# Kernel optimization log

Measured on AMD Instinct MI355X. Metric: run time of the kernel, lower is better.

Reference implementation:

```python
import jax, jax.numpy as jnp
import numpy as np

B, C, H, W = 16, 256, 64, 64
K, HID, ITERS, EPS = 4, 512, 3, 1e-8


def _ln(x, g, b, eps=1e-5):
    m = jnp.mean(x, axis=-1, keepdims=True)
    v = jnp.mean((x - m) ** 2, axis=-1, keepdims=True)
    return (x - m) * jax.lax.rsqrt(v + eps) * g + b


def setup_inputs() -> dict:
    key = jax.random.key(0)
    ks = jax.random.split(key, 24)

    def lin(k, o, i):
        lim = np.sqrt(6.0 / (o + i)).astype(np.float32)
        return jax.random.uniform(k, (o, i), jnp.float32, -lim, lim)

    return {
        "x": jax.random.normal(ks[0], (B, C, H, W), jnp.float32),
        "noise": jax.random.normal(ks[1], (B, K, C), jnp.float32),
        "slot_mu": jax.random.normal(ks[2], (1, 1, C), jnp.float32),
        "slot_log_sigma": jnp.zeros((1, 1, C), jnp.float32),
        "ln_in_g": jnp.ones((C,)), "ln_in_b": jnp.zeros((C,)),
        "ln_sl_g": jnp.ones((C,)), "ln_sl_b": jnp.zeros((C,)),
        "ln_mlp_g": jnp.ones((C,)), "ln_mlp_b": jnp.zeros((C,)),
        "Wq": lin(ks[3], C, C), "bq": jnp.zeros((C,)),
        "Wk": lin(ks[4], C, C), "bk": jnp.zeros((C,)),
        "Wv": lin(ks[5], C, C), "bv": jnp.zeros((C,)),
        "Wu": lin(ks[6], C, 2 * C), "bu": jnp.zeros((C,)),
        "W1": lin(ks[7], HID, C), "b1": jnp.zeros((HID,)),
        "W2": lin(ks[8], C, HID), "b2": jnp.zeros((C,)),
        "We1": lin(ks[9], C // 2, C), "be1": jnp.zeros((C // 2,)),
        "We2": lin(ks[10], 1, C // 2), "be2": jnp.zeros((1,)),
    }


def reference(x, noise, slot_mu, slot_log_sigma, ln_in_g, ln_in_b, ln_sl_g, ln_sl_b,
              ln_mlp_g, ln_mlp_b, Wq, bq, Wk, bk, Wv, bv, Wu, bu, W1, b1, W2, b2,
              We1, be1, We2, be2):
    # b c h w -> b (h w) c
    xn = x.reshape(B, C, H * W).transpose(0, 2, 1)
    xn = _ln(xn, ln_in_g, ln_in_b)
    # k, v depend only on xn; hoisted out of the loop (same math)
    k = jnp.einsum('bnc,dc->bnd', xn, Wk) + bk
    v = jnp.einsum('bnc,dc->bnd', xn, Wv) + bv
    scale = C ** (-0.5)
    slots = slot_mu + jnp.exp(slot_log_sigma) * noise
    for _ in range(ITERS):
        prev = slots
        s = _ln(slots, ln_sl_g, ln_sl_b)
        q = jnp.einsum('bkc,dc->bkd', s, Wq) + bq
        attn = jax.nn.softmax(jnp.einsum('bkc,bnc->bkn', q, k) * scale, axis=1)
        w = attn / (jnp.sum(attn, axis=-1, keepdims=True) + EPS)
        updates = jnp.einsum('bkn,bnc->bkc', w, v)
        combined = jnp.concatenate([prev, updates], axis=-1)  # (B,K,2C)
        slots = jnp.einsum('bkc,dc->bkd', combined, Wu) + bu + prev
        m = _ln(slots, ln_mlp_g, ln_mlp_b)
        h = jax.nn.gelu(jnp.einsum('bkc,hc->bkh', m, W1) + b1, approximate=False)
        slots = slots + jnp.einsum('bkh,ch->bkc', h, W2) + b2
    e = jax.nn.gelu(jnp.einsum('bkc,dc->bkd', slots, We1) + be1, approximate=False)
    slot_weights = jax.nn.sigmoid(jnp.einsum('bkd,od->bko', e, We2) + be2)[..., 0]
    return slots, slot_weights
```

## Files before the change

kernel.cpp:

```cpp
#include <hip/hip_runtime.h>
#include <math.h>

#define B_    16
#define C_    256
#define NPIX  4096
#define K_    4
#define HID_  512
#define ITERS_ 3
#define NROWS (B_*NPIX)
#define EPS_  1e-8f

__device__ __forceinline__ float gelu_f(float x) {
    return 0.5f * x * (1.0f + erff(x * 0.70710678118654752f));
}

__device__ __forceinline__ unsigned short f2bf(float x) {
    union { float f; unsigned u; } v; v.f = x;
    unsigned r = v.u + 0x7fffu + ((v.u >> 16) & 1u);
    return (unsigned short)(r >> 16);
}
__device__ __forceinline__ float bflo(unsigned u) {
    union { unsigned u; float f; } v; v.u = u << 16; return v.f;
}
__device__ __forceinline__ float bfhi(unsigned u) {
    union { unsigned u; float f; } v; v.u = u & 0xffff0000u; return v.f;
}
__device__ __forceinline__ float4 shfl_xor4(float4 v, int m) {
    v.x = __shfl_xor(v.x, m); v.y = __shfl_xor(v.y, m);
    v.z = __shfl_xor(v.z, m); v.w = __shfl_xor(v.w, m);
    return v;
}
__device__ __forceinline__ void fma4(float4& a, const float4 w, const float4 s) {
    a.x = fmaf(w.x, s.x, a.x); a.y = fmaf(w.y, s.y, a.y);
    a.z = fmaf(w.z, s.z, a.z); a.w = fmaf(w.w, s.w, a.w);
}
__device__ __forceinline__ float hsum4(const float4 a) {
    return (a.x + a.y) + (a.z + a.w);
}

__device__ __forceinline__ void redpair256(float a, float b, int tid, int q,
                                           float* r8, float& o1, float& o2) {
    if (q == 0) {
        #pragma unroll
        for (int m = 1; m <= 32; m <<= 1) { a += __shfl_xor(a, m); b += __shfl_xor(b, m); }
        if ((tid & 63) == 0) { r8[(tid >> 6) * 2] = a; r8[(tid >> 6) * 2 + 1] = b; }
    }
    __syncthreads();
    o1 = r8[0] + r8[2] + r8[4] + r8[6];
    o2 = r8[1] + r8[3] + r8[5] + r8[7];
    __syncthreads();
}

__global__ __launch_bounds__(256) void prep_pack_kernel(
    const float* __restrict__ Wu, const float* __restrict__ W1,
    const float* __restrict__ W2, const float* __restrict__ We1,
    const float* __restrict__ Wq, const float* __restrict__ bk,
    const float* __restrict__ bq,
    float4* __restrict__ WuC4, float4* __restrict__ W14,
    float4* __restrict__ W24, float4* __restrict__ We14,
    float* __restrict__ wqoff) {
    __shared__ float r4[4];
    int i = blockIdx.x * 256 + threadIdx.x;
    if (blockIdx.x == 352) {
        int c = threadIdx.x;
        float s = 0.f;
        for (int dd = 0; dd < 256; ++dd) s = fmaf(Wq[dd * 256 + c], bk[dd], s);
        wqoff[c] = s;
        float p = bq[c] * bk[c];
        #pragma unroll
        for (int m = 1; m <= 32; m <<= 1) p += __shfl_xor(p, m);
        if ((c & 63) == 0) r4[c >> 6] = p;
        __syncthreads();
        if (c == 0) wqoff[256] = r4[0] + r4[1] + r4[2] + r4[3];
        return;
    }
    if (i < 16384) {
        int c4 = i >> 8, dd = i & 255;
        WuC4[i] = *(const float4*)&Wu[dd * 512 + c4 * 4];
    } else if (i < 49152) {
        int j = i - 16384; int c4 = j >> 9, h = j & 511;
        W14[j] = *(const float4*)&W1[h * 256 + c4 * 4];
    } else if (i < 81920) {
        int j = i - 49152; int h4 = j >> 8, dd = j & 255;
        W24[j] = *(const float4*)&W2[dd * 512 + h4 * 4];
    } else {
        int j = i - 81920; int c4 = j >> 7, e = j & 127;
        We14[j] = *(const float4*)&We1[e * 256 + c4 * 4];
    }
}

__global__ __launch_bounds__(256) void prep_compose_kernel(
    const float* __restrict__ Wu, const float* __restrict__ Wv,
    const float* __restrict__ Wk, const float* __restrict__ Wq,
    const float* __restrict__ bv, const float* __restrict__ bq,
    float4* __restrict__ WuC4, float4* __restrict__ Wqk4,
    float* __restrict__ bv2, float* __restrict__ bqk) {
    __shared__ float wur[256], wkc[256];
    __shared__ float ldsA[256], ldsB[256];
    __shared__ float r1[4], r2[4];
    const int d = blockIdx.x, c = threadIdx.x;
    wur[c] = Wu[d * 512 + 256 + c];
    wkc[c] = Wk[c * 256 + d];
    __syncthreads();
    float a = 0.f, b = 0.f;
    #pragma unroll 4
    for (int e = 0; e < 256; ++e) {
        a = fmaf(wur[e], Wv[e * 256 + c], a);
        b = fmaf(wkc[e], Wq[e * 256 + c], b);
    }
    ldsA[c] = a; ldsB[c] = b;
    float p1 = wur[c] * bv[c], p2 = wkc[c] * bq[c];
    #pragma unroll
    for (int m = 1; m <= 32; m <<= 1) { p1 += __shfl_xor(p1, m); p2 += __shfl_xor(p2, m); }
    if ((c & 63) == 0) { r1[c >> 6] = p1; r2[c >> 6] = p2; }
    __syncthreads();
    if (c < 64) {
        float4 qa = { ldsA[4 * c], ldsA[4 * c + 1], ldsA[4 * c + 2], ldsA[4 * c + 3] };
        float4 qb = { ldsB[4 * c], ldsB[4 * c + 1], ldsB[4 * c + 2], ldsB[4 * c + 3] };
        WuC4[(64 + c) * 256 + d] = qa;
        Wqk4[c * 256 + d] = qb;
    }
    if (c == 0) {
        bv2[d] = r1[0] + r1[1] + r1[2] + r1[3];
        bqk[d] = r2[0] + r2[1] + r2[2] + r2[3];
    }
}

__global__ __launch_bounds__(256) void xn_fused_kernel(
    const float* __restrict__ x, const float* __restrict__ g, const float* __restrict__ bta,
    unsigned short* __restrict__ xnb) {
    __shared__ float tile[256][65];
    __shared__ float sg[256], sb[256];
    __shared__ float red1[256], red2[256];
    __shared__ float smean[64], srstd[64];
    const int tid = threadIdx.x;
    const int nt = blockIdx.x << 6, b = blockIdx.y;

    sg[tid] = g[tid]; sb[tid] = bta[tid];
    #pragma unroll
    for (int r = 0; r < 64; ++r) {
        int idx = tid + (r << 8);
        int c_l = idx >> 6, n_l = idx & 63;
        tile[c_l][n_l] = x[(size_t)(b * C_ + c_l) * NPIX + nt + n_l];
    }
    __syncthreads();
    {
        int cq = tid >> 6, n_l = tid & 63;
        float s = 0.f, s2 = 0.f;
        #pragma unroll 8
        for (int c = cq * 64; c < cq * 64 + 64; ++c) {
            float v = tile[c][n_l];
            s += v; s2 += v * v;
        }
        red1[tid] = s; red2[tid] = s2;
    }
    __syncthreads();
    if (tid < 64) {
        float s  = red1[tid] + red1[tid + 64] + red1[tid + 128] + red1[tid + 192];
        float s2 = red2[tid] + red2[tid + 64] + red2[tid + 128] + red2[tid + 192];
        float m = s * (1.0f / C_);
        smean[tid] = m;
        srstd[tid] = rsqrtf(s2 * (1.0f / C_) - m * m + 1e-5f);
    }
    __syncthreads();
    #pragma unroll
    for (int r = 0; r < 32; ++r) {
        int idx = tid + (r << 8);
        int n_l = idx >> 7, cp = idx & 127;
        int c0 = cp << 1;
        float mn = smean[n_l], rs = srstd[n_l];
        float v0 = (tile[c0][n_l] - mn) * rs * sg[c0] + sb[c0];
        float v1 = (tile[c0 + 1][n_l] - mn) * rs * sg[c0 + 1] + sb[c0 + 1];
        ushort2 o; o.x = f2bf(v0); o.y = f2bf(v1);
        *reinterpret_cast<ushort2*>(&xnb[((size_t)(b * NPIX + nt + n_l)) * C_ + c0]) = o;
    }
}


__device__ __forceinline__ void ln_qt_1024(
    float v, int tid, int d, int q, int r,
    const float* __restrict__ g_sl, const float* __restrict__ b_sl,
    const float4* __restrict__ Wqk4, const float* __restrict__ bqk,
    const float* __restrict__ wqoff,
    float* __restrict__ qtbuf, float* __restrict__ qoffbuf,
    float* snorm, float* pq, float* r8) {
    float a = (q == 0) ? v : 0.f;
    float sm, s2;
    redpair256(a, a * v, tid, q, r8, sm, s2);
    if (q == 0) {
        float m = sm * (1.f / C_);
        float rs = rsqrtf(s2 * (1.f / C_) - m * m + 1e-5f);
        snorm[d] = (v - m) * rs * g_sl[d] + b_sl[d];
    }
    __syncthreads();
    {
        const float4* sn4 = (const float4*)snorm;
        float4 a0 = {0,0,0,0}, a1 = {0,0,0,0};
        int c4b = q << 4;
        #pragma unroll
        for (int i = 0; i < 16; i += 2) {
            fma4(a0, Wqk4[(c4b + i) * 256 + d], sn4[c4b + i]);
            fma4(a1, Wqk4[(c4b + i + 1) * 256 + d], sn4[c4b + i + 1]);
        }
        pq[q * 256 + d] = hsum4(a0) + hsum4(a1);
    }
    float p = (q == 0) ? snorm[d] * wqoff[d] : 0.f;
    float qo, dum;
    redpair256(p, 0.f, tid, q, r8, qo, dum);
    if (tid == 0) qoffbuf[r] = qo + wqoff[256];
    if (q == 0)
        qtbuf[r * C_ + d] = pq[d] + pq[256 + d] + pq[512 + d] + pq[768 + d] + bqk[d];
}

__global__ __launch_bounds__(1024) void slot_init_q_kernel(
    const float* __restrict__ noise, const float* __restrict__ mu,
    const float* __restrict__ log_sigma,
    const float* __restrict__ g_sl, const float* __restrict__ b_sl,
    const float4* __restrict__ Wqk4, const float* __restrict__ bqk,
    const float* __restrict__ wqoff,
    float* __restrict__ slots, float* __restrict__ qtbuf, float* __restrict__ qoffbuf,
    float* __restrict__ usum, float* __restrict__ denom) {
    __shared__ __align__(16) float snorm[256];
    __shared__ float pq[1024];
    __shared__ float r8[8];
    int tid = threadIdx.x;
    int d = tid & 255, q = tid >> 8;
    int r = blockIdx.x;
    float v = 0.f;
    if (q == 0) {
        v = mu[d] + expf(log_sigma[d]) * noise[r * C_ + d];
        slots[r * C_ + d] = v;
        usum[r * C_ + d] = 0.f;
    }
    if (tid == 0) denom[r] = 0.f;
    ln_qt_1024(v, tid, d, q, r, g_sl, b_sl, Wqk4, bqk, wqoff,
               qtbuf, qoffbuf, snorm, pq, r8);
}

__device__ __forceinline__ float slot_update_body(
    int tid, int d, int q, int r, const float* __restrict__ slots,
    float* __restrict__ usum, float* __restrict__ denom,
    const float* __restrict__ bv2,
    const float4* __restrict__ WuC4, const float* __restrict__ bu,
    const float* __restrict__ g_mlp, const float* __restrict__ b_mlp,
    const float4* __restrict__ W14, const float* __restrict__ b1,
    const float4* __restrict__ W24, const float* __restrict__ b2,
    float* comb, float* pq, float* mrow, float* hrow,
    float* r8, float* s_denom, float* s_scale) {
    float uv = 0.f, prev = 0.f;
    if (q == 0) {
        uv = usum[r * C_ + d];
        usum[r * C_ + d] = 0.f;
        prev = slots[r * C_ + d];
    }
    if (tid == 0) {
        float dv = denom[r];
        *s_denom = dv + EPS_;
        *s_scale = dv / (dv + EPS_);
        denom[r] = 0.f;
    }
    __syncthreads();
    if (q == 0) {
        comb[d] = prev;
        comb[256 + d] = uv / *s_denom;
    }
    __syncthreads();
    const float4* cb4 = (const float4*)comb;
    {
        float4 a0 = {0,0,0,0}, a1 = {0,0,0,0}, a2 = {0,0,0,0}, a3 = {0,0,0,0};
        int c4b = q << 5;
        #pragma unroll
        for (int i = 0; i < 32; i += 4) {
            float4 w0 = WuC4[(c4b + i + 0) * 256 + d];
            float4 w1 = WuC4[(c4b + i + 1) * 256 + d];
            float4 w2 = WuC4[(c4b + i + 2) * 256 + d];
            float4 w3 = WuC4[(c4b + i + 3) * 256 + d];
            fma4(a0, w0, cb4[c4b + i + 0]); fma4(a1, w1, cb4[c4b + i + 1]);
            fma4(a2, w2, cb4[c4b + i + 2]); fma4(a3, w3, cb4[c4b + i + 3]);
        }
        pq[q * 256 + d] = (hsum4(a0) + hsum4(a1)) + (hsum4(a2) + hsum4(a3));
    }
    __syncthreads();
    float nv = 0.f, aa = 0.f;
    if (q == 0) {
        nv = pq[d] + pq[256 + d] + pq[512 + d] + pq[768 + d]
           + bu[d] + prev + (*s_scale) * bv2[d];
        aa = nv;
    }
    float sm, s2;
    redpair256(aa, aa * nv, tid, q, r8, sm, s2);
    if (q == 0) {
        float m = sm * (1.f / C_);
        float rs = rsqrtf(s2 * (1.f / C_) - m * m + 1e-5f);
        mrow[d] = (nv - m) * rs * g_mlp[d] + b_mlp[d];
    }
    __syncthreads();
    const float4* m4 = (const float4*)mrow;
    {
        int j = tid & 511, h2 = tid >> 9;
        float4 a0 = {0,0,0,0}, a1 = {0,0,0,0};
        int c4b = h2 << 5;
        #pragma unroll
        for (int i = 0; i < 32; i += 2) {
            float4 w0 = W14[(c4b + i + 0) * 512 + j];
            float4 w1 = W14[(c4b + i + 1) * 512 + j];
            fma4(a0, w0, m4[c4b + i + 0]); fma4(a1, w1, m4[c4b + i + 1]);
        }
        pq[h2 * 512 + j] = hsum4(a0) + hsum4(a1);
    }
    __syncthreads();
    if (tid < 512) hrow[tid] = gelu_f(pq[tid] + pq[512 + tid] + b1[tid]);
    __syncthreads();
    const float4* h4 = (const float4*)hrow;
    {
        float4 a0 = {0,0,0,0}, a1 = {0,0,0,0}, a2 = {0,0,0,0}, a3 = {0,0,0,0};
        int h4b = q << 5;
        #pragma unroll
        for (int i = 0; i < 32; i += 4) {
            float4 w0 = W24[(h4b + i + 0) * 256 + d];
            float4 w1 = W24[(h4b + i + 1) * 256 + d];
            float4 w2 = W24[(h4b + i + 2) * 256 + d];
            float4 w3 = W24[(h4b + i + 3) * 256 + d];
            fma4(a0, w0, h4[h4b + i + 0]); fma4(a1, w1, h4[h4b + i + 1]);
            fma4(a2, w2, h4[h4b + i + 2]); fma4(a3, w3, h4[h4b + i + 3]);
        }
        pq[q * 256 + d] = (hsum4(a0) + hsum4(a1)) + (hsum4(a2) + hsum4(a3));
    }
    __syncthreads();
    float ov = 0.f;
    if (q == 0)
        ov = nv + pq[d] + pq[256 + d] + pq[512 + d] + pq[768 + d] + b2[d];
    return ov;
}

__global__ __launch_bounds__(1024) void slot_update_q_kernel(
    float* __restrict__ slots, float* __restrict__ usum, float* __restrict__ denom,
    const float* __restrict__ bv2,
    const float4* __restrict__ WuC4, const float* __restrict__ bu,
    const float* __restrict__ g_mlp, const float* __restrict__ b_mlp,
    const float4* __restrict__ W14, const float* __restrict__ b1,
    const float4* __restrict__ W24, const float* __restrict__ b2,
    const float* __restrict__ g_sl, const float* __restrict__ b_sl,
    const float4* __restrict__ Wqk4, const float* __restrict__ bqk,
    const float* __restrict__ wqoff,
    float* __restrict__ qtbuf, float* __restrict__ qoffbuf) {
    __shared__ __align__(16) float comb[512];
    __shared__ __align__(16) float mrow[256];
    __shared__ __align__(16) float hrow[512];
    __shared__ float pq[1024];
    __shared__ float r8[8];
    __shared__ float s_denom, s_scale;
    int tid = threadIdx.x;
    int d = tid & 255, q = tid >> 8;
    int r = blockIdx.x;
    float ov = slot_update_body(tid, d, q, r, slots, usum, denom, bv2, WuC4, bu,
                                g_mlp, b_mlp, W14, b1, W24, b2,
                                comb, pq, mrow, hrow, r8, &s_denom, &s_scale);
    if (q == 0) slots[r * C_ + d] = ov;
    ln_qt_1024(ov, tid, d, q, r, g_sl, b_sl, Wqk4, bqk, wqoff,
               qtbuf, qoffbuf, mrow, pq, r8);
}

__global__ __launch_bounds__(1024) void slot_update_final_kernel(
    float* __restrict__ slots, float* __restrict__ usum, float* __restrict__ denom,
    const float* __restrict__ bv2,
    const float4* __restrict__ WuC4, const float* __restrict__ bu,
    const float* __restrict__ g_mlp, const float* __restrict__ b_mlp,
    const float4* __restrict__ W14, const float* __restrict__ b1,
    const float4* __restrict__ W24, const float* __restrict__ b2,
    const float4* __restrict__ We14, const float* __restrict__ be1,
    const float* __restrict__ We2, const float* __restrict__ be2,
    float* __restrict__ out) {
    __shared__ __align__(16) float comb[512];
    __shared__ __align__(16) float mrow[256];
    __shared__ __align__(16) float hrow[512];
    __shared__ float pq[1024];
    __shared__ float r8[8];
    __shared__ float s_denom, s_scale;
    __shared__ float erow[128];
    int tid = threadIdx.x;
    int d = tid & 255, q = tid >> 8;
    int r = blockIdx.x;
    float ov = slot_update_body(tid, d, q, r, slots, usum, denom, bv2, WuC4, bu,
                                g_mlp, b_mlp, W14, b1, W24, b2,
                                comb, pq, mrow, hrow, r8, &s_denom, &s_scale);
    if (q == 0) {
        out[r * C_ + d] = ov;
        mrow[d] = ov;
    }
    __syncthreads();
    const float4* m4 = (const float4*)mrow;
    {
        int e = tid & 127, o8 = tid >> 7;
        float4 a0 = {0,0,0,0}, a1 = {0,0,0,0};
        int c4b = o8 << 3;
        #pragma unroll
        for (int i = 0; i < 8; i += 2) {
            fma4(a0, We14[(c4b + i) * 128 + e], m4[c4b + i]);
            fma4(a1, We14[(c4b + i + 1) * 128 + e], m4[c4b + i + 1]);
        }
        pq[o8 * 128 + e] = hsum4(a0) + hsum4(a1);
    }
    __syncthreads();
    if (tid < 128) {
        float s = 0.f;
        #pragma unroll
        for (int o = 0; o < 8; ++o) s += pq[o * 128 + tid];
        erow[tid] = gelu_f(s + be1[tid]);
    }
    __syncthreads();
    if (tid < 64) {
        float p = We2[tid] * erow[tid] + We2[tid + 64] * erow[tid + 64];
        #pragma unroll
        for (int m = 1; m <= 32; m <<= 1) p += __shfl_xor(p, m);
        if (tid == 0) out[B_ * K_ * C_ + r] = 1.0f / (1.0f + expf(-(p + be2[0])));
    }
}

__global__ __launch_bounds__(256) void attn_fused_kernel(
    const float* __restrict__ qtbuf, const float* __restrict__ qoffbuf,
    const unsigned short* __restrict__ xnb,
    float* __restrict__ usum, float* __restrict__ denom) {
    __shared__ float4 qT[264];
    __shared__ float attns[K_][64];
    __shared__ float upd_s[K_][256];
    __shared__ float asw[4][4];
    __shared__ float4 qo_s;

    const int tid = threadIdx.x;
    const int b = blockIdx.y;
    const int chunk = blockIdx.x;
    const int n0 = chunk << 6;
    const int wave = tid >> 6, lane = tid & 63;

    {
        int c = tid;
        float4 qv;
        qv.x = qtbuf[b * 1024 + c];
        qv.y = qtbuf[b * 1024 + 256 + c];
        qv.z = qtbuf[b * 1024 + 512 + c];
        qv.w = qtbuf[b * 1024 + 768 + c];
        qT[c + (c >> 5)] = qv;
        if (tid == 0) qo_s = *(const float4*)&qoffbuf[b * 4];
    }
    __syncthreads();

    const int cpart = tid & 7;
    const int npair = tid >> 3;
    const int c0 = cpart << 5;
    float4 acc0 = {0.f, 0.f, 0.f, 0.f}, acc1 = {0.f, 0.f, 0.f, 0.f};
    const unsigned short* kbase = xnb + ((size_t)b * NPIX + n0 + npair * 2) * C_ + c0;
    #pragma unroll
    for (int j = 0; j < 4; ++j) {
        uint4 k0 = *reinterpret_cast<const uint4*>(kbase + j * 8);
        uint4 k1 = *reinterpret_cast<const uint4*>(kbase + C_ + j * 8);
        const unsigned kw0[4] = {k0.x, k0.y, k0.z, k0.w};
        const unsigned kw1[4] = {k1.x, k1.y, k1.z, k1.w};
        #pragma unroll
        for (int jj = 0; jj < 4; ++jj) {
            int cidx = c0 + j * 8 + jj * 2 + cpart;
            float4 qa = qT[cidx];
            float4 qb = qT[cidx + 1];
            float f00 = bflo(kw0[jj]), f01 = bfhi(kw0[jj]);
            float f10 = bflo(kw1[jj]), f11 = bfhi(kw1[jj]);
            acc0.x += f00 * qa.x + f01 * qb.x;  acc0.y += f00 * qa.y + f01 * qb.y;
            acc0.z += f00 * qa.z + f01 * qb.z;  acc0.w += f00 * qa.w + f01 * qb.w;
            acc1.x += f10 * qa.x + f11 * qb.x;  acc1.y += f10 * qa.y + f11 * qb.y;
            acc1.z += f10 * qa.z + f11 * qb.z;  acc1.w += f10 * qa.w + f11 * qb.w;
        }
    }
    #pragma unroll
    for (int m = 1; m <= 4; m <<= 1) {
        acc0 = acc0 + shfl_xor4(acc0, m);
        acc1 = acc1 + shfl_xor4(acc1, m);
    }
    float4 w0, w1;
    {
        float4 l = (acc0 + qo_s) * 0.0625f;
        float mx = fmaxf(fmaxf(l.x, l.y), fmaxf(l.z, l.w));
        w0.x = expf(l.x - mx); w0.y = expf(l.y - mx);
        w0.z = expf(l.z - mx); w0.w = expf(l.w - mx);
        float inv = 1.0f / (w0.x + w0.y + w0.z + w0.w);
        w0 = w0 * inv;
        l = (acc1 + qo_s) * 0.0625f;
        mx = fmaxf(fmaxf(l.x, l.y), fmaxf(l.z, l.w));
        w1.x = expf(l.x - mx); w1.y = expf(l.y - mx);
        w1.z = expf(l.z - mx); w1.w = expf(l.w - mx);
        inv = 1.0f / (w1.x + w1.y + w1.z + w1.w);
        w1 = w1 * inv;
    }
    if (cpart == 0) {
        int n_l = npair * 2;
        attns[0][n_l] = w0.x; attns[1][n_l] = w0.y; attns[2][n_l] = w0.z; attns[3][n_l] = w0.w;
        attns[0][n_l + 1] = w1.x; attns[1][n_l + 1] = w1.y;
        attns[2][n_l + 1] = w1.z; attns[3][n_l + 1] = w1.w;
    }
    float4 ws = w0 + w1;
    #pragma unroll
    for (int m = 8; m <= 32; m <<= 1) ws = ws + shfl_xor4(ws, m);
    if (lane == 0) {
        asw[wave][0] = ws.x; asw[wave][1] = ws.y; asw[wave][2] = ws.z; asw[wave][3] = ws.w;
    }
    __syncthreads();
    if (tid < 4)
        atomicAdd(&denom[b * 4 + tid],
                  asw[0][tid] + asw[1][tid] + asw[2][tid] + asw[3][tid]);

    const int h = wave >> 1;
    const int chalf = (wave & 1) << 7;
    const int c = chalf + lane * 2;
    float a0[K_] = {0.f, 0.f, 0.f, 0.f};
    float a1[K_] = {0.f, 0.f, 0.f, 0.f};
    const unsigned short* vbase = xnb + ((size_t)b * NPIX + n0 + h * 32) * C_ + c;
    #pragma unroll 4
    for (int nn = 0; nn < 32; ++nn) {
        unsigned vv = *reinterpret_cast<const unsigned*>(vbase + (size_t)nn * C_);
        float v0 = bflo(vv), v1 = bfhi(vv);
        int n_l = h * 32 + nn;
        float q0 = attns[0][n_l], q1 = attns[1][n_l], q2 = attns[2][n_l], q3 = attns[3][n_l];
        a0[0] = fmaf(q0, v0, a0[0]); a1[0] = fmaf(q0, v1, a1[0]);
        a0[1] = fmaf(q1, v0, a0[1]); a1[1] = fmaf(q1, v1, a1[1]);
        a0[2] = fmaf(q2, v0, a0[2]); a1[2] = fmaf(q2, v1, a1[2]);
        a0[3] = fmaf(q3, v0, a0[3]); a1[3] = fmaf(q3, v1, a1[3]);
    }
    __syncthreads();
    if (h == 0) {
        #pragma unroll
        for (int k = 0; k < K_; ++k) { upd_s[k][c] = a0[k]; upd_s[k][c + 1] = a1[k]; }
    }
    __syncthreads();
    if (h == 1) {
        #pragma unroll
        for (int k = 0; k < K_; ++k) { upd_s[k][c] += a0[k]; upd_s[k][c + 1] += a1[k]; }
    }
    __syncthreads();
    #pragma unroll
    for (int k = 0; k < K_; ++k)
        atomicAdd(&usum[((size_t)b * K_ + k) * 256 + tid], upd_s[k][tid]);
}

extern "C" void kernel_launch(void* const* d_in, const int* in_sizes, int n_in,
                              void* d_out, int out_size, void* d_ws, size_t ws_size,
                              hipStream_t stream) {
    (void)in_sizes; (void)n_in; (void)out_size; (void)ws_size;
    const float* x        = (const float*)d_in[0];
    const float* noise    = (const float*)d_in[1];
    const float* slot_mu  = (const float*)d_in[2];
    const float* slot_ls  = (const float*)d_in[3];
    const float* ln_in_g  = (const float*)d_in[4];
    const float* ln_in_b  = (const float*)d_in[5];
    const float* ln_sl_g  = (const float*)d_in[6];
    const float* ln_sl_b  = (const float*)d_in[7];
    const float* ln_mlp_g = (const float*)d_in[8];
    const float* ln_mlp_b = (const float*)d_in[9];
    const float* Wq = (const float*)d_in[10];
    const float* bq = (const float*)d_in[11];
    const float* Wk = (const float*)d_in[12];
    const float* bk = (const float*)d_in[13];
    const float* Wv = (const float*)d_in[14];
    const float* bv = (const float*)d_in[15];
    const float* Wu = (const float*)d_in[16];
    const float* bu = (const float*)d_in[17];
    const float* W1 = (const float*)d_in[18];
    const float* b1 = (const float*)d_in[19];
    const float* W2 = (const float*)d_in[20];
    const float* b2 = (const float*)d_in[21];
    const float* We1 = (const float*)d_in[22];
    const float* be1 = (const float*)d_in[23];
    const float* We2 = (const float*)d_in[24];
    const float* be2 = (const float*)d_in[25];
    float* out = (float*)d_out;

    char* ws = (char*)d_ws;
    unsigned short* xnb = (unsigned short*)ws;
    float4* WuC4 = (float4*)(xnb + (size_t)NROWS * C_);
    float4* W14  = WuC4 + 32768;
    float4* W24  = W14 + 32768;
    float4* We14 = W24 + 32768;
    float4* Wqk4 = We14 + 8192;
    float* bv2   = (float*)(Wqk4 + 16384);
    float* bqk   = bv2 + 256;
    float* wqoff = bqk + 256;
    float* slots = wqoff + 260;
    float* qtbuf = slots + B_ * K_ * C_;
    float* qoffb = qtbuf + B_ * K_ * C_;
    float* usum  = qoffb + B_ * K_;
    float* denom = usum + B_ * K_ * C_;

    prep_pack_kernel<<<353, 256, 0, stream>>>(Wu, W1, W2, We1, Wq, bk, bq,
                                              WuC4, W14, W24, We14, wqoff);
    prep_compose_kernel<<<256, 256, 0, stream>>>(Wu, Wv, Wk, Wq, bv, bq,
                                                 WuC4, Wqk4, bv2, bqk);
    xn_fused_kernel<<<dim3(64, 16), 256, 0, stream>>>(x, ln_in_g, ln_in_b, xnb);
    slot_init_q_kernel<<<B_ * K_, 1024, 0, stream>>>(noise, slot_mu, slot_ls,
                                                     ln_sl_g, ln_sl_b, Wqk4, bqk, wqoff,
                                                     slots, qtbuf, qoffb, usum, denom);
    for (int it = 0; it < ITERS_; ++it) {
        attn_fused_kernel<<<dim3(64, 16), 256, 0, stream>>>(qtbuf, qoffb, xnb,
                                                            usum, denom);
        if (it < ITERS_ - 1) {
            slot_update_q_kernel<<<B_ * K_, 1024, 0, stream>>>(
                slots, usum, denom, bv2, WuC4, bu, ln_mlp_g, ln_mlp_b,
                W14, b1, W24, b2, ln_sl_g, ln_sl_b, Wqk4, bqk, wqoff, qtbuf, qoffb);
        } else {
            slot_update_final_kernel<<<B_ * K_, 1024, 0, stream>>>(
                slots, usum, denom, bv2, WuC4, bu, ln_mlp_g, ln_mlp_b,
                W14, b1, W24, b2, We14, be1, We2, be2, out);
        }
    }
}
```

Baseline: 307.0 us.

## Split per-slot update into multiple wider-grid kernels over output columns

Result: faster. 299.0 us (-2.6%).

```diff
diff --git a/kernel.cpp b/kernel.cpp
--- a/kernel.cpp
+++ b/kernel.cpp
@@ -38,17 +38,14 @@
     return (a.x + a.y) + (a.z + a.w);
 }
 
-__device__ __forceinline__ void redpair256(float a, float b, int tid, int q,
-                                           float* r8, float& o1, float& o2) {
-    if (q == 0) {
-        #pragma unroll
-        for (int m = 1; m <= 32; m <<= 1) { a += __shfl_xor(a, m); b += __shfl_xor(b, m); }
-        if ((tid & 63) == 0) { r8[(tid >> 6) * 2] = a; r8[(tid >> 6) * 2 + 1] = b; }
-    }
+__device__ __forceinline__ void redpair256t(float a, float b, int t, float* r8,
+                                            float& o1, float& o2) {
+    #pragma unroll
+    for (int m = 1; m <= 32; m <<= 1) { a += __shfl_xor(a, m); b += __shfl_xor(b, m); }
+    if ((t & 63) == 0) { r8[(t >> 6) * 2] = a; r8[(t >> 6) * 2 + 1] = b; }
     __syncthreads();
     o1 = r8[0] + r8[2] + r8[4] + r8[6];
     o2 = r8[1] + r8[3] + r8[5] + r8[7];
-    __syncthreads();
 }
 
 __global__ __launch_bounds__(256) void prep_pack_kernel(
@@ -177,244 +174,209 @@
 }
 
 
-__device__ __forceinline__ void ln_qt_1024(
-    float v, int tid, int d, int q, int r,
-    const float* __restrict__ g_sl, const float* __restrict__ b_sl,
-    const float4* __restrict__ Wqk4, const float* __restrict__ bqk,
-    const float* __restrict__ wqoff,
-    float* __restrict__ qtbuf, float* __restrict__ qoffbuf,
-    float* snorm, float* pq, float* r8) {
-    float a = (q == 0) ? v : 0.f;
-    float sm, s2;
-    redpair256(a, a * v, tid, q, r8, sm, s2);
-    if (q == 0) {
-        float m = sm * (1.f / C_);
-        float rs = rsqrtf(s2 * (1.f / C_) - m * m + 1e-5f);
-        snorm[d] = (v - m) * rs * g_sl[d] + b_sl[d];
-    }
-    __syncthreads();
-    {
-        const float4* sn4 = (const float4*)snorm;
-        float4 a0 = {0,0,0,0}, a1 = {0,0,0,0};
-        int c4b = q << 4;
-        #pragma unroll
-        for (int i = 0; i < 16; i += 2) {
-            fma4(a0, Wqk4[(c4b + i) * 256 + d], sn4[c4b + i]);
-            fma4(a1, Wqk4[(c4b + i + 1) * 256 + d], sn4[c4b + i + 1]);
-        }
-        pq[q * 256 + d] = hsum4(a0) + hsum4(a1);
-    }
-    float p = (q == 0) ? snorm[d] * wqoff[d] : 0.f;
-    float qo, dum;
-    redpair256(p, 0.f, tid, q, r8, qo, dum);
-    if (tid == 0) qoffbuf[r] = qo + wqoff[256];
-    if (q == 0)
-        qtbuf[r * C_ + d] = pq[d] + pq[256 + d] + pq[512 + d] + pq[768 + d] + bqk[d];
-}
-
-__global__ __launch_bounds__(1024) void slot_init_q_kernel(
+__global__ __launch_bounds__(256) void init_slots_kernel(
     const float* __restrict__ noise, const float* __restrict__ mu,
     const float* __restrict__ log_sigma,
-    const float* __restrict__ g_sl, const float* __restrict__ b_sl,
-    const float4* __restrict__ Wqk4, const float* __restrict__ bqk,
-    const float* __restrict__ wqoff,
-    float* __restrict__ slots, float* __restrict__ qtbuf, float* __restrict__ qoffbuf,
-    float* __restrict__ usum, float* __restrict__ denom) {
-    __shared__ __align__(16) float snorm[256];
-    __shared__ float pq[1024];
-    __shared__ float r8[8];
-    int tid = threadIdx.x;
-    int d = tid & 255, q = tid >> 8;
-    int r = blockIdx.x;
-    float v = 0.f;
-    if (q == 0) {
-        v = mu[d] + expf(log_sigma[d]) * noise[r * C_ + d];
-        slots[r * C_ + d] = v;
-        usum[r * C_ + d] = 0.f;
-    }
-    if (tid == 0) denom[r] = 0.f;
-    ln_qt_1024(v, tid, d, q, r, g_sl, b_sl, Wqk4, bqk, wqoff,
-               qtbuf, qoffbuf, snorm, pq, r8);
-}
-
-__device__ __forceinline__ float slot_update_body(
-    int tid, int d, int q, int r, const float* __restrict__ slots,
-    float* __restrict__ usum, float* __restrict__ denom,
-    const float* __restrict__ bv2,
-    const float4* __restrict__ WuC4, const float* __restrict__ bu,
-    const float* __restrict__ g_mlp, const float* __restrict__ b_mlp,
-    const float4* __restrict__ W14, const float* __restrict__ b1,
-    const float4* __restrict__ W24, const float* __restrict__ b2,
-    float* comb, float* pq, float* mrow, float* hrow,
-    float* r8, float* s_denom, float* s_scale) {
-    float uv = 0.f, prev = 0.f;
-    if (q == 0) {
-        uv = usum[r * C_ + d];
-        usum[r * C_ + d] = 0.f;
-        prev = slots[r * C_ + d];
-    }
-    if (tid == 0) {
-        float dv = denom[r];
-        *s_denom = dv + EPS_;
-        *s_scale = dv / (dv + EPS_);
-        denom[r] = 0.f;
-    }
-    __syncthreads();
-    if (q == 0) {
-        comb[d] = prev;
-        comb[256 + d] = uv / *s_denom;
-    }
-    __syncthreads();
-    const float4* cb4 = (const float4*)comb;
-    {
-        float4 a0 = {0,0,0,0}, a1 = {0,0,0,0}, a2 = {0,0,0,0}, a3 = {0,0,0,0};
-        int c4b = q << 5;
-        #pragma unroll
-        for (int i = 0; i < 32; i += 4) {
-            float4 w0 = WuC4[(c4b + i + 0) * 256 + d];
-            float4 w1 = WuC4[(c4b + i + 1) * 256 + d];
-            float4 w2 = WuC4[(c4b + i + 2) * 256 + d];
-            float4 w3 = WuC4[(c4b + i + 3) * 256 + d];
-            fma4(a0, w0, cb4[c4b + i + 0]); fma4(a1, w1, cb4[c4b + i + 1]);
-            fma4(a2, w2, cb4[c4b + i + 2]); fma4(a3, w3, cb4[c4b + i + 3]);
-        }
-        pq[q * 256 + d] = (hsum4(a0) + hsum4(a1)) + (hsum4(a2) + hsum4(a3));
-    }
-    __syncthreads();
-    float nv = 0.f, aa = 0.f;
-    if (q == 0) {
-        nv = pq[d] + pq[256 + d] + pq[512 + d] + pq[768 + d]
-           + bu[d] + prev + (*s_scale) * bv2[d];
-        aa = nv;
-    }
-    float sm, s2;
-    redpair256(aa, aa * nv, tid, q, r8, sm, s2);
-    if (q == 0) {
-        float m = sm * (1.f / C_);
-        float rs = rsqrtf(s2 * (1.f / C_) - m * m + 1e-5f);
-        mrow[d] = (nv - m) * rs * g_mlp[d] + b_mlp[d];
-    }
-    __syncthreads();
-    const float4* m4 = (const float4*)mrow;
-    {
-        int j = tid & 511, h2 = tid >> 9;
-        float4 a0 = {0,0,0,0}, a1 = {0,0,0,0};
-        int c4b = h2 << 5;
-        #pragma unroll
-        for (int i = 0; i < 32; i += 2) {
-            float4 w0 = W14[(c4b + i + 0) * 512 + j];
-            float4 w1 = W14[(c4b + i + 1) * 512 + j];
-            fma4(a0, w0, m4[c4b + i + 0]); fma4(a1, w1, m4[c4b + i + 1]);
-        }
-        pq[h2 * 512 + j] = hsum4(a0) + hsum4(a1);
-    }
-    __syncthreads();
-    if (tid < 512) hrow[tid] = gelu_f(pq[tid] + pq[512 + tid] + b1[tid]);
-    __syncthreads();
-    const float4* h4 = (const float4*)hrow;
-    {
-        float4 a0 = {0,0,0,0}, a1 = {0,0,0,0}, a2 = {0,0,0,0}, a3 = {0,0,0,0};
-        int h4b = q << 5;
-        #pragma unroll
-        for (int i = 0; i < 32; i += 4) {
-            float4 w0 = W24[(h4b + i + 0) * 256 + d];
-            float4 w1 = W24[(h4b + i + 1) * 256 + d];
-            float4 w2 = W24[(h4b + i + 2) * 256 + d];
-            float4 w3 = W24[(h4b + i + 3) * 256 + d];
-            fma4(a0, w0, h4[h4b + i + 0]); fma4(a1, w1, h4[h4b + i + 1]);
-            fma4(a2, w2, h4[h4b + i + 2]); fma4(a3, w3, h4[h4b + i + 3]);
-        }
-        pq[q * 256 + d] = (hsum4(a0) + hsum4(a1)) + (hsum4(a2) + hsum4(a3));
-    }
-    __syncthreads();
-    float ov = 0.f;
-    if (q == 0)
-        ov = nv + pq[d] + pq[256 + d] + pq[512 + d] + pq[768 + d] + b2[d];
-    return ov;
-}
-
-__global__ __launch_bounds__(1024) void slot_update_q_kernel(
-    float* __restrict__ slots, float* __restrict__ usum, float* __restrict__ denom,
-    const float* __restrict__ bv2,
-    const float4* __restrict__ WuC4, const float* __restrict__ bu,
-    const float* __restrict__ g_mlp, const float* __restrict__ b_mlp,
-    const float4* __restrict__ W14, const float* __restrict__ b1,
-    const float4* __restrict__ W24, const float* __restrict__ b2,
+    float* __restrict__ slots, float* __restrict__ usum, float* __restrict__ denom) {
+    int t = threadIdx.x, r = blockIdx.x;
+    float v = mu[t] + expf(log_sigma[t]) * noise[r * C_ + t];
+    slots[r * C_ + t] = v;
+    usum[r * C_ + t] = 0.f;
+    if (t == 0) denom[r] = 0.f;
+}
+
+__global__ __launch_bounds__(256) void qt_kernel(
+    const float* __restrict__ src,
     const float* __restrict__ g_sl, const float* __restrict__ b_sl,
     const float4* __restrict__ Wqk4, const float* __restrict__ bqk,
     const float* __restrict__ wqoff,
     float* __restrict__ qtbuf, float* __restrict__ qoffbuf) {
+    __shared__ __align__(16) float snorm[256];
+    __shared__ float pq[256];
+    __shared__ float r8[8];
+    const int t = threadIdx.x, dq = blockIdx.x, r = blockIdx.y;
+    float v = src[r * C_ + t];
+    float sm, s2;
+    redpair256t(v, v * v, t, r8, sm, s2);
+    float mean = sm * (1.f / C_);
+    float rs = rsqrtf(s2 * (1.f / C_) - mean * mean + 1e-5f);
+    snorm[t] = (v - mean) * rs * g_sl[t] + b_sl[t];
+    __syncthreads();
+    const float4* sn4 = (const float4*)snorm;
+    const int dloc = t & 63, ks = t >> 6;
+    const int d = dq * 64 + dloc;
+    {
+        float4 a0 = {0,0,0,0}, a1 = {0,0,0,0};
+        int c4b = ks << 4;
+        #pragma unroll
+        for (int i = 0; i < 16; i += 2) {
+            fma4(a0, Wqk4[(c4b + i) * 256 + d], sn4[c4b + i]);
+            fma4(a1, Wqk4[(c4b + i + 1) * 256 + d], sn4[c4b + i + 1]);
+        }
+        pq[ks * 64 + dloc] = hsum4(a0) + hsum4(a1);
+    }
+    __syncthreads();
+    if (t < 64) {
+        float s = pq[t] + pq[64 + t] + pq[128 + t] + pq[192 + t];
+        qtbuf[r * C_ + dq * 64 + t] = s + bqk[dq * 64 + t];
+    }
+    if (dq == 0) {
+        float p = snorm[t] * wqoff[t];
+        #pragma unroll
+        for (int m = 1; m <= 32; m <<= 1) p += __shfl_xor(p, m);
+        if ((t & 63) == 0) r8[t >> 6] = p;
+        __syncthreads();
+        if (t == 0) qoffbuf[r] = r8[0] + r8[1] + r8[2] + r8[3] + wqoff[256];
+    }
+}
+
+__global__ __launch_bounds__(256) void upd_wu_kernel(
+    const float* __restrict__ slots, const float* __restrict__ usum,
+    const float* __restrict__ denom,
+    const float4* __restrict__ WuC4, const float* __restrict__ bu,
+    const float* __restrict__ bv2,
+    float* __restrict__ nvbuf) {
     __shared__ __align__(16) float comb[512];
-    __shared__ __align__(16) float mrow[256];
-    __shared__ __align__(16) float hrow[512];
-    __shared__ float pq[1024];
-    __shared__ float r8[8];
-    __shared__ float s_denom, s_scale;
-    int tid = threadIdx.x;
-    int d = tid & 255, q = tid >> 8;
-    int r = blockIdx.x;
-    float ov = slot_update_body(tid, d, q, r, slots, usum, denom, bv2, WuC4, bu,
-                                g_mlp, b_mlp, W14, b1, W24, b2,
-                                comb, pq, mrow, hrow, r8, &s_denom, &s_scale);
-    if (q == 0) slots[r * C_ + d] = ov;
-    ln_qt_1024(ov, tid, d, q, r, g_sl, b_sl, Wqk4, bqk, wqoff,
-               qtbuf, qoffbuf, mrow, pq, r8);
-}
-
-__global__ __launch_bounds__(1024) void slot_update_final_kernel(
-    float* __restrict__ slots, float* __restrict__ usum, float* __restrict__ denom,
-    const float* __restrict__ bv2,
-    const float4* __restrict__ WuC4, const float* __restrict__ bu,
+    __shared__ float pq[256];
+    __shared__ float sden, sscale;
+    const int t = threadIdx.x, dq = blockIdx.x, r = blockIdx.y;
+    if (t == 0) { float dv = denom[r]; sden = dv + EPS_; sscale = dv / (dv + EPS_); }
+    comb[t] = slots[r * C_ + t];
+    float uv = usum[r * C_ + t];
+    __syncthreads();
+    comb[256 + t] = uv / sden;
+    __syncthreads();
+    const float4* cb4 = (const float4*)comb;
+    const int dloc = t & 31, ks = t >> 5;
+    const int d = dq * 32 + dloc;
+    {
+        float4 a0 = {0,0,0,0}, a1 = {0,0,0,0};
+        int c4b = ks << 4;
+        #pragma unroll
+        for (int i = 0; i < 16; i += 2) {
+            fma4(a0, WuC4[(c4b + i) * 256 + d], cb4[c4b + i]);
+            fma4(a1, WuC4[(c4b + i + 1) * 256 + d], cb4[c4b + i + 1]);
+        }
+        pq[ks * 32 + dloc] = hsum4(a0) + hsum4(a1);
+    }
+    __syncthreads();
+    if (t < 32) {
+        int dd = dq * 32 + t;
+        float s = 0.f;
+        #pragma unroll
+        for (int i = 0; i < 8; ++i) s += pq[i * 32 + t];
+        nvbuf[r * C_ + dd] = s + bu[dd] + comb[dd] + sscale * bv2[dd];
+    }
+}
+
+__global__ __launch_bounds__(256) void upd_w1_kernel(
+    const float* __restrict__ nvbuf,
     const float* __restrict__ g_mlp, const float* __restrict__ b_mlp,
     const float4* __restrict__ W14, const float* __restrict__ b1,
+    float* __restrict__ hbuf, float* __restrict__ usum, float* __restrict__ denom) {
+    __shared__ __align__(16) float mrow[256];
+    __shared__ float pq[256];
+    __shared__ float r8[8];
+    const int t = threadIdx.x, hq = blockIdx.x, r = blockIdx.y;
+    float nv = nvbuf[r * C_ + t];
+    float sm, s2;
+    redpair256t(nv, nv * nv, t, r8, sm, s2);
+    float mean = sm * (1.f / C_);
+    float rs = rsqrtf(s2 * (1.f / C_) - mean * mean + 1e-5f);
+    mrow[t] = (nv - mean) * rs * g_mlp[t] + b_mlp[t];
+    if (hq == 0) {
+        usum[r * C_ + t] = 0.f;
+        if (t == 0) denom[r] = 0.f;
+    }
+    __syncthreads();
+    const float4* m4 = (const float4*)mrow;
+    const int hloc = t & 63, ks = t >> 6;
+    const int h = hq * 64 + hloc;
+    {
+        float4 a0 = {0,0,0,0}, a1 = {0,0,0,0};
+        int c4b = ks << 4;
+        #pragma unroll
+        for (int i = 0; i < 16; i += 2) {
+            fma4(a0, W14[(c4b + i) * 512 + h], m4[c4b + i]);
+            fma4(a1, W14[(c4b + i + 1) * 512 + h], m4[c4b + i + 1]);
+        }
+        pq[ks * 64 + hloc] = hsum4(a0) + hsum4(a1);
+    }
+    __syncthreads();
+    if (t < 64) {
+        float s = pq[t] + pq[64 + t] + pq[128 + t] + pq[192 + t];
+        hbuf[r * HID_ + hq * 64 + t] = gelu_f(s + b1[hq * 64 + t]);
+    }
+}
+
+__global__ __launch_bounds__(256) void upd_w2_kernel(
+    const float* __restrict__ nvbuf, const float* __restrict__ hbuf,
     const float4* __restrict__ W24, const float* __restrict__ b2,
+    float* __restrict__ dst) {
+    __shared__ __align__(16) float hrow[512];
+    __shared__ float pq[256];
+    const int t = threadIdx.x, dq = blockIdx.x, r = blockIdx.y;
+    hrow[t] = hbuf[r * HID_ + t];
+    hrow[256 + t] = hbuf[r * HID_ + 256 + t];
+    __syncthreads();
+    const float4* h4 = (const float4*)hrow;
+    const int dloc = t & 31, ks = t >> 5;
+    const int d = dq * 32 + dloc;
+    {
+        float4 a0 = {0,0,0,0}, a1 = {0,0,0,0};
+        int h4b = ks << 4;
+        #pragma unroll
+        for (int i = 0; i < 16; i += 2) {
+            fma4(a0, W24[(h4b + i) * 256 + d], h4[h4b + i]);
+            fma4(a1, W24[(h4b + i + 1) * 256 + d], h4[h4b + i + 1]);
+        }
+        pq[ks * 32 + dloc] = hsum4(a0) + hsum4(a1);
+    }
+    __syncthreads();
+    if (t < 32) {
+        int dd = dq * 32 + t;
+        float s = 0.f;
+        #pragma unroll
+        for (int i = 0; i < 8; ++i) s += pq[i * 32 + t];
+        dst[r * C_ + dd] = nvbuf[r * C_ + dd] + s + b2[dd];
+    }
+}
+
+__global__ __launch_bounds__(256) void head_kernel(
+    const float* __restrict__ ovbuf,
     const float4* __restrict__ We14, const float* __restrict__ be1,
     const float* __restrict__ We2, const float* __restrict__ be2,
     float* __restrict__ out) {
-    __shared__ __align__(16) float comb[512];
     __shared__ __align__(16) float mrow[256];
-    __shared__ __align__(16) float hrow[512];
-    __shared__ float pq[1024];
-    __shared__ float r8[8];
-    __shared__ float s_denom, s_scale;
+    __shared__ float pq[256];
     __shared__ float erow[128];
-    int tid = threadIdx.x;
-    int d = tid & 255, q = tid >> 8;
-    int r = blockIdx.x;
-    float ov = slot_update_body(tid, d, q, r, slots, usum, denom, bv2, WuC4, bu,
-                                g_mlp, b_mlp, W14, b1, W24, b2,
-                                comb, pq, mrow, hrow, r8, &s_denom, &s_scale);
-    if (q == 0) {
-        out[r * C_ + d] = ov;
-        mrow[d] = ov;
-    }
+    __shared__ float r4[4];
+    const int t = threadIdx.x, r = blockIdx.x;
+    mrow[t] = ovbuf[r * C_ + t];
     __syncthreads();
     const float4* m4 = (const float4*)mrow;
-    {
-        int e = tid & 127, o8 = tid >> 7;
+    const int e = t & 127, o2 = t >> 7;
+    {
         float4 a0 = {0,0,0,0}, a1 = {0,0,0,0};
-        int c4b = o8 << 3;
-        #pragma unroll
-        for (int i = 0; i < 8; i += 2) {
+        int c4b = o2 << 5;
+        #pragma unroll
+        for (int i = 0; i < 32; i += 2) {
             fma4(a0, We14[(c4b + i) * 128 + e], m4[c4b + i]);
             fma4(a1, We14[(c4b + i + 1) * 128 + e], m4[c4b + i + 1]);
         }
-        pq[o8 * 128 + e] = hsum4(a0) + hsum4(a1);
-    }
-    __syncthreads();
-    if (tid < 128) {
-        float s = 0.f;
-        #pragma unroll
-        for (int o = 0; o < 8; ++o) s += pq[o * 128 + tid];
-        erow[tid] = gelu_f(s + be1[tid]);
-    }
-    __syncthreads();
-    if (tid < 64) {
-        float p = We2[tid] * erow[tid] + We2[tid + 64] * erow[tid + 64];
+        pq[o2 * 128 + e] = hsum4(a0) + hsum4(a1);
+    }
+    __syncthreads();
+    if (t < 128) erow[t] = gelu_f(pq[t] + pq[128 + t] + be1[t]);
+    __syncthreads();
+    if (t < 64) {
+        float p = We2[t] * erow[t] + We2[t + 64] * erow[t + 64];
         #pragma unroll
         for (int m = 1; m <= 32; m <<= 1) p += __shfl_xor(p, m);
-        if (tid == 0) out[B_ * K_ * C_ + r] = 1.0f / (1.0f + expf(-(p + be2[0])));
-    }
+        if (t == 0) { r4[0] = p; }
+    }
+    __syncthreads();
+    if (t == 0) out[B_ * K_ * C_ + r] = 1.0f / (1.0f + expf(-(r4[0] + be2[0])));
 }
 
 __global__ __launch_bounds__(256) void attn_fused_kernel(
@@ -586,26 +548,30 @@
     float* qoffb = qtbuf + B_ * K_ * C_;
     float* usum  = qoffb + B_ * K_;
     float* denom = usum + B_ * K_ * C_;
+    float* nvbuf = denom + B_ * K_;
+    float* hbuf  = nvbuf + B_ * K_ * C_;
 
     prep_pack_kernel<<<353, 256, 0, stream>>>(Wu, W1, W2, We1, Wq, bk, bq,
                                               WuC4, W14, W24, We14, wqoff);
     prep_compose_kernel<<<256, 256, 0, stream>>>(Wu, Wv, Wk, Wq, bv, bq,
                                                  WuC4, Wqk4, bv2, bqk);
     xn_fused_kernel<<<dim3(64, 16), 256, 0, stream>>>(x, ln_in_g, ln_in_b, xnb);
-    slot_init_q_kernel<<<B_ * K_, 1024, 0, stream>>>(noise, slot_mu, slot_ls,
-                                                     ln_sl_g, ln_sl_b, Wqk4, bqk, wqoff,
-                                                     slots, qtbuf, qoffb, usum, denom);
+    init_slots_kernel<<<B_ * K_, 256, 0, stream>>>(noise, slot_mu, slot_ls,
+                                                   slots, usum, denom);
+    qt_kernel<<<dim3(4, B_ * K_), 256, 0, stream>>>(slots, ln_sl_g, ln_sl_b,
+                                                    Wqk4, bqk, wqoff, qtbuf, qoffb);
     for (int it = 0; it < ITERS_; ++it) {
         attn_fused_kernel<<<dim3(64, 16), 256, 0, stream>>>(qtbuf, qoffb, xnb,
                                                             usum, denom);
-        if (it < ITERS_ - 1) {
-            slot_update_q_kernel<<<B_ * K_, 1024, 0, stream>>>(
-                slots, usum, denom, bv2, WuC4, bu, ln_mlp_g, ln_mlp_b,
-                W14, b1, W24, b2, ln_sl_g, ln_sl_b, Wqk4, bqk, wqoff, qtbuf, qoffb);
-        } else {
-            slot_update_final_kernel<<<B_ * K_, 1024, 0, stream>>>(
-                slots, usum, denom, bv2, WuC4, bu, ln_mlp_g, ln_mlp_b,
-                W14, b1, W24, b2, We14, be1, We2, be2, out);
-        }
-    }
-}
+        upd_wu_kernel<<<dim3(8, B_ * K_), 256, 0, stream>>>(slots, usum, denom,
+                                                            WuC4, bu, bv2, nvbuf);
+        upd_w1_kernel<<<dim3(8, B_ * K_), 256, 0, stream>>>(nvbuf, ln_mlp_g, ln_mlp_b,
+                                                            W14, b1, hbuf, usum, denom);
+        upd_w2_kernel<<<dim3(8, B_ * K_), 256, 0, stream>>>(
+            nvbuf, hbuf, W24, b2, (it < ITERS_ - 1) ? slots : out);
+        if (it < ITERS_ - 1)
+            qt_kernel<<<dim3(4, B_ * K_), 256, 0, stream>>>(slots, ln_sl_g, ln_sl_b,
+                                                            Wqk4, bqk, wqoff, qtbuf, qoffb);
+    }
+    head_kernel<<<B_ * K_, 256, 0, stream>>>(out, We14, be1, We2, be2, out);
+}
```
